# Kernel tuning notes

Hardware: AMD Instinct MI355X
Metric: run time of the kernel (lower is better)

The kernel has to match this reference:

```python
import jax, jax.numpy as jnp
import numpy as np

MAX_DELTAS = 4  # number of concurrently loaded delta adapters


def _dequant(qw, qz, sc):
    """GPTQ-style 4-bit dequant with a single group (g_idx == 0).

    qw: [D, O, K//8] int32, 8 x 4-bit values packed along the input (K) dim.
    qz: [D, O//8, 1] int32, 8 x 4-bit zero points packed along the output dim.
    sc: [D, O, 1] float scales (one group).
    Returns dense delta weights [D, O, K].
    """
    shifts = jnp.arange(8, dtype=jnp.int32) * 4
    D, O, Kp = qw.shape
    w = ((qw[:, :, :, None] >> shifts) & 0xF).reshape(D, O, Kp * 8)   # [D,O,K]
    z = ((qz[:, :, 0][:, :, None] >> shifts) & 0xF).reshape(D, O)     # [D,O]
    return (w.astype(sc.dtype) - (z.astype(sc.dtype) + 1.0)[:, :, None]) * sc


def setup_inputs() -> dict:
    key = jax.random.key(0)
    ks = jax.random.split(key, 16)
    T, IN = 1024, 4096
    Q, KV = 4096, 1024  # 32 q-heads, 8 kv-heads, head_size 128
    OUT = Q + 2 * KV    # 6144
    D, PACK = MAX_DELTAS, 8
    IMAX = np.int32(2**31 - 1)
    return {
        "x": jax.random.normal(ks[0], (T, IN), dtype=jnp.float32),
        "w_base": jax.random.normal(ks[1], (OUT, IN), dtype=jnp.float32) * 0.02,
        "bias": jax.random.normal(ks[2], (OUT,), dtype=jnp.float32) * 0.02,
        "qweight_q": jax.random.randint(ks[3], (D, Q, IN // PACK), 0, IMAX, dtype=jnp.int32),
        "qweight_k": jax.random.randint(ks[4], (D, KV, IN // PACK), 0, IMAX, dtype=jnp.int32),
        "qweight_v": jax.random.randint(ks[5], (D, KV, IN // PACK), 0, IMAX, dtype=jnp.int32),
        "qzeros_q": jax.random.randint(ks[6], (D, Q // PACK, 1), 0, IMAX, dtype=jnp.int32),
        "qzeros_k": jax.random.randint(ks[7], (D, KV // PACK, 1), 0, IMAX, dtype=jnp.int32),
        "qzeros_v": jax.random.randint(ks[8], (D, KV // PACK, 1), 0, IMAX, dtype=jnp.int32),
        "scales_q": jax.random.uniform(ks[9], (D, Q, 1), dtype=jnp.float32) * 0.01,
        "scales_k": jax.random.uniform(ks[10], (D, KV, 1), dtype=jnp.float32) * 0.01,
        "scales_v": jax.random.uniform(ks[11], (D, KV, 1), dtype=jnp.float32) * 0.01,
        "indices": jax.random.randint(ks[12], (T,), 0, D, dtype=jnp.int32),
    }


def reference(x, w_base, bias, qweight_q, qweight_k, qweight_v,
              qzeros_q, qzeros_k, qzeros_v, scales_q, scales_k, scales_v,
              indices):
    # Base fused QKV projection.
    out = x @ w_base.T + bias  # [T, OUT]
    # Dequantize the three packed delta stacks and concatenate along out dim,
    # matching the (q, k, v) output_slices scatter of apply_delta.
    Wd = jnp.concatenate([
        _dequant(qweight_q, qzeros_q, scales_q),
        _dequant(qweight_k, qzeros_k, scales_k),
        _dequant(qweight_v, qzeros_v, scales_v),
    ], axis=1)  # [D, OUT, IN]
    # Per-token indexed delta matmul: token t uses adapter indices[t].
    for d in range(MAX_DELTAS):
        xm = jnp.where((indices == d)[:, None], x, 0.0)  # [T, IN]
        out = out + xm @ Wd[d].T
    return out
```

## Files before the change

kernel.cpp:

```cpp
#include <hip/hip_runtime.h>
#include <stdint.h>

#define T_TOK 1024
#define K_IN  4096
#define N_OUT 6144
#define N_Q   4096
#define N_KV  1024
#define N_D   4
#define KP    512

#define TM 128
#define TN 128
#define BK 64
#define KSPLIT 2
#define KHALF (K_IN / KSPLIT)
#define PM_MAX 1536
#define MT (PM_MAX/TM)
#define NT (N_OUT/TN)

typedef __attribute__((ext_vector_type(8)))  short  short8;
typedef __attribute__((ext_vector_type(4)))  float  float4v;

__device__ __forceinline__ ushort f2bf(float f) {
    uint32_t u = __float_as_uint(f);
    u = (u + 0x7FFFu + ((u >> 16) & 1u)) >> 16;
    return (ushort)u;
}
__device__ __forceinline__ uint pack2(ushort a, ushort b) {
    return (uint)a | ((uint)b << 16);
}

__global__ void build_perm_kernel(const int* __restrict__ indices,
                                  int* __restrict__ perm,
                                  int* __restrict__ pofs) {
    __shared__ int cnt[N_D], cur[N_D], ps[N_D + 1];
    int tid = threadIdx.x;
    if (tid < N_D) { cnt[tid] = 0; cur[tid] = 0; }
    __syncthreads();
    for (int t = tid; t < T_TOK; t += blockDim.x) atomicAdd(&cnt[indices[t]], 1);
    for (int p = tid; p < PM_MAX; p += blockDim.x) perm[p] = -1;
    __syncthreads();
    if (tid == 0) {
        int run = 0;
        for (int d = 0; d < N_D; d++) { ps[d] = run; run += ((cnt[d] + TM - 1) / TM) * TM; }
        ps[N_D] = run;
        for (int d = 0; d <= N_D; d++) pofs[d] = ps[d];
    }
    __syncthreads();
    for (int t = tid; t < T_TOK; t += blockDim.x) {
        int d = indices[t];
        int r = atomicAdd(&cur[d], 1);
        perm[ps[d] + r] = t;
    }
}

__global__ void dequant_wall_kernel(const float* __restrict__ w_base,
                                    const int* __restrict__ qw_q, const int* __restrict__ qw_k, const int* __restrict__ qw_v,
                                    const int* __restrict__ qz_q, const int* __restrict__ qz_k, const int* __restrict__ qz_v,
                                    const float* __restrict__ sc_q, const float* __restrict__ sc_k, const float* __restrict__ sc_v,
                                    ushort* __restrict__ wall) {
    int id  = blockIdx.x * blockDim.x + threadIdx.x;
    int kq  = id & (KP - 1);
    int o   = id >> 9;

    const int* qw; const int* qz; const float* sc; int r, Osec;
    if (o < N_Q)            { qw = qw_q; qz = qz_q; sc = sc_q; r = o;                Osec = N_Q;  }
    else if (o < N_Q + N_KV){ qw = qw_k; qz = qz_k; sc = sc_k; r = o - N_Q;          Osec = N_KV; }
    else                    { qw = qw_v; qz = qz_v; sc = sc_v; r = o - (N_Q + N_KV); Osec = N_KV; }

    const float* wbp = w_base + (size_t)o * K_IN + (size_t)kq * 8;
    float4 wb0 = *(const float4*)(wbp);
    float4 wb1 = *(const float4*)(wbp + 4);
    float wb[8] = {wb0.x, wb0.y, wb0.z, wb0.w, wb1.x, wb1.y, wb1.z, wb1.w};

#pragma unroll
    for (int d = 0; d < N_D; d++) {
        int   q  = qw[((size_t)d * Osec + r) * KP + kq];
        int   zq = qz[(size_t)d * (Osec / 8) + (r >> 3)];
        float s  = sc[(size_t)d * Osec + r];
        float zs = (float)(((zq >> ((r & 7) * 4)) & 0xF) + 1) * s;

        ushort res[8];
#pragma unroll
        for (int j = 0; j < 8; j++) {
            float v = wb[j] + (float)((q >> (4 * j)) & 0xF) * s - zs;
            res[j] = f2bf(v);
        }
        uint4 packv;
        packv.x = pack2(res[0], res[1]); packv.y = pack2(res[2], res[3]);
        packv.z = pack2(res[4], res[5]); packv.w = pack2(res[6], res[7]);
        *(uint4*)(wall + ((size_t)d * N_OUT + o) * K_IN + (size_t)kq * 8) = packv;
    }
}

__global__ void build_xp_kernel(const float* __restrict__ x,
                                const int* __restrict__ perm,
                                ushort* __restrict__ xp) {
    int pm = blockIdx.x;
    int c0 = blockIdx.y * 2048 + threadIdx.x * 8;
    int tok = perm[pm];
    ushort res[8];
    if (tok < 0) {
#pragma unroll
        for (int j = 0; j < 8; j++) res[j] = 0;
    } else {
        const float* src = x + (size_t)tok * K_IN + c0;
#pragma unroll
        for (int j = 0; j < 8; j++) res[j] = f2bf(src[j]);
    }
    uint4 packv;
    packv.x = pack2(res[0], res[1]); packv.y = pack2(res[2], res[3]);
    packv.z = pack2(res[4], res[5]); packv.w = pack2(res[6], res[7]);
    *(uint4*)(xp + (size_t)pm * K_IN + c0) = packv;
}

__global__ void init_out_kernel(const float* __restrict__ bias,
                                float* __restrict__ out) {
    int id = blockIdx.x * blockDim.x + threadIdx.x;
    int n4 = id & (N_OUT / 4 - 1);
    int t  = id / (N_OUT / 4);
    float4 b = *(const float4*)(bias + n4 * 4);
    *(float4*)(out + (size_t)t * N_OUT + n4 * 4) = b;
}

__global__ __launch_bounds__(256, 4) void gemm_kernel(
    const ushort* __restrict__ xp, const ushort* __restrict__ wall,
    const int* __restrict__ perm, const int* __restrict__ pofs,
    float* __restrict__ out) {

    __shared__ ushort As[TM * BK];
    __shared__ ushort Bs[TN * BK];

    int bn = blockIdx.x, bm = blockIdx.y, kz = blockIdx.z;
    int m0 = bm * TM, n0 = bn * TN;
    int ptot = pofs[N_D];
    if (m0 >= ptot) return;
    int d = 0;
    while (d < N_D - 1 && m0 >= pofs[d + 1]) d++;

    const ushort* wsec = wall + (size_t)d * N_OUT * K_IN;

    int tid  = threadIdx.x;
    int lane = tid & 63;
    int wv   = tid >> 6;
    int wm   = (wv & 1) * 64;
    int wn   = (wv >> 1) * 64;
    int quad = lane >> 4;
    int l16  = lane & 15;
    int xa   = l16 & 7;

    const float4v zero4 = {0.f, 0.f, 0.f, 0.f};
    float4v acc[4][4];
#pragma unroll
    for (int i = 0; i < 4; i++)
#pragma unroll
        for (int j = 0; j < 4; j++) acc[i][j] = zero4;

    int kbase = kz * KHALF;
    for (int k0 = kbase; k0 < kbase + KHALF; k0 += BK) {
#pragma unroll
        for (int w = 0; w < 4; w++) {
            int p   = w * 256 + tid;
            int row = p >> 3;
            int ckl = (p & 7) ^ (row & 7);
            const ushort* ga = xp   + (size_t)(m0 + row) * K_IN + k0 + ckl * 8;
            const ushort* gb = wsec + (size_t)(n0 + row) * K_IN + k0 + ckl * 8;
            int base = (w * 256 + (tid & ~63)) * 8;
            __builtin_amdgcn_global_load_lds((const __attribute__((address_space(1))) void*)ga,
                                             (__attribute__((address_space(3))) void*)(As + base), 16, 0, 0);
            __builtin_amdgcn_global_load_lds((const __attribute__((address_space(1))) void*)gb,
                                             (__attribute__((address_space(3))) void*)(Bs + base), 16, 0, 0);
        }
        __syncthreads();

#pragma unroll
        for (int kk = 0; kk < BK; kk += 32) {
            int ckb = (kk >> 3) + quad;
            short8 a[4], b[4];
#pragma unroll
            for (int i = 0; i < 4; i++)
                a[i] = *(const short8*)(As + (wm + i * 16 + l16) * BK + (ckb ^ xa) * 8);
#pragma unroll
            for (int j = 0; j < 4; j++)
                b[j] = *(const short8*)(Bs + (wn + j * 16 + l16) * BK + (ckb ^ xa) * 8);
#pragma unroll
            for (int i = 0; i < 4; i++)
#pragma unroll
                for (int j = 0; j < 4; j++)
                    acc[i][j] = __builtin_amdgcn_mfma_f32_16x16x32_bf16(a[i], b[j], acc[i][j], 0, 0, 0);
        }
        __syncthreads();
    }

#pragma unroll
    for (int i = 0; i < 4; i++) {
        int toks[4];
#pragma unroll
        for (int r = 0; r < 4; r++) toks[r] = perm[m0 + wm + i * 16 + quad * 4 + r];
#pragma unroll
        for (int j = 0; j < 4; j++) {
            int col = n0 + wn + j * 16 + l16;
#pragma unroll
            for (int r = 0; r < 4; r++) {
                int tok = toks[r];
                if (tok >= 0) atomicAdd(out + (size_t)tok * N_OUT + col, acc[i][j][r]);
            }
        }
    }
}

extern "C" void kernel_launch(void* const* d_in, const int* in_sizes, int n_in,
                              void* d_out, int out_size, void* d_ws, size_t ws_size,
                              hipStream_t stream) {
    const float* x      = (const float*)d_in[0];
    const float* w_base = (const float*)d_in[1];
    const float* bias   = (const float*)d_in[2];
    const int*   qw_q   = (const int*)d_in[3];
    const int*   qw_k   = (const int*)d_in[4];
    const int*   qw_v   = (const int*)d_in[5];
    const int*   qz_q   = (const int*)d_in[6];
    const int*   qz_k   = (const int*)d_in[7];
    const int*   qz_v   = (const int*)d_in[8];
    const float* sc_q   = (const float*)d_in[9];
    const float* sc_k   = (const float*)d_in[10];
    const float* sc_v   = (const float*)d_in[11];
    const int*   indices= (const int*)d_in[12];
    float* out = (float*)d_out;

    char* ws = (char*)d_ws;
    ushort* wall = (ushort*)ws;
    size_t wall_bytes = (size_t)N_D * N_OUT * K_IN * 2;
    ushort* xp = (ushort*)(ws + wall_bytes);
    size_t xp_bytes = (size_t)PM_MAX * K_IN * 2;
    int* perm = (int*)(ws + wall_bytes + xp_bytes);
    int* pofs = perm + PM_MAX;

    build_perm_kernel<<<1, 256, 0, stream>>>(indices, perm, pofs);
    dequant_wall_kernel<<<(N_OUT * KP) / 256, 256, 0, stream>>>(
        w_base, qw_q, qw_k, qw_v, qz_q, qz_k, qz_v, sc_q, sc_k, sc_v, wall);
    build_xp_kernel<<<dim3(PM_MAX, 2), 256, 0, stream>>>(x, perm, xp);
    init_out_kernel<<<(T_TOK * N_OUT / 4) / 256, 256, 0, stream>>>(bias, out);
    gemm_kernel<<<dim3(NT, MT, KSPLIT), 256, 0, stream>>>(xp, wall, perm, pofs, out);
}
```

Baseline: 376.9 us.

## Double-buffer GEMM LDS tiles, swizzle block order, use nontemporal loads

The GEMM now stages the next K-tile into a second LDS buffer while computing on the current one, which halves barriers per step and overlaps global loads with MFMA work. The grid is flattened and remapped so groups of 8 adjacent N-tiles are scheduled together for L2 reuse of activation tiles. The dequant and activation-cast kernels use nontemporal loads for streamed inputs. LDS usage doubles, so occupancy is lowered to 2 blocks per CU.

```diff
diff --git a/kernel.cpp b/kernel.cpp
--- a/kernel.cpp
+++ b/kernel.cpp
@@ -14,12 +14,16 @@
 #define BK 64
 #define KSPLIT 2
 #define KHALF (K_IN / KSPLIT)
+#define NSTEPS (KHALF / BK)
 #define PM_MAX 1536
 #define MT (PM_MAX/TM)
 #define NT (N_OUT/TN)
+#define NBLK (NT * MT * KSPLIT)
 
 typedef __attribute__((ext_vector_type(8)))  short  short8;
 typedef __attribute__((ext_vector_type(4)))  float  float4v;
+typedef __attribute__((ext_vector_type(4)))  float  f32x4;
+typedef __attribute__((ext_vector_type(4)))  uint   u32x4;
 
 __device__ __forceinline__ ushort f2bf(float f) {
     uint32_t u = __float_as_uint(f);
@@ -68,14 +72,14 @@
     else if (o < N_Q + N_KV){ qw = qw_k; qz = qz_k; sc = sc_k; r = o - N_Q;          Osec = N_KV; }
     else                    { qw = qw_v; qz = qz_v; sc = sc_v; r = o - (N_Q + N_KV); Osec = N_KV; }
 
-    const float* wbp = w_base + (size_t)o * K_IN + (size_t)kq * 8;
-    float4 wb0 = *(const float4*)(wbp);
-    float4 wb1 = *(const float4*)(wbp + 4);
+    const f32x4* wbp = (const f32x4*)(w_base + (size_t)o * K_IN + (size_t)kq * 8);
+    f32x4 wb0 = __builtin_nontemporal_load(wbp);
+    f32x4 wb1 = __builtin_nontemporal_load(wbp + 1);
     float wb[8] = {wb0.x, wb0.y, wb0.z, wb0.w, wb1.x, wb1.y, wb1.z, wb1.w};
 
 #pragma unroll
     for (int d = 0; d < N_D; d++) {
-        int   q  = qw[((size_t)d * Osec + r) * KP + kq];
+        int   q  = __builtin_nontemporal_load(qw + ((size_t)d * Osec + r) * KP + kq);
         int   zq = qz[(size_t)d * (Osec / 8) + (r >> 3)];
         float s  = sc[(size_t)d * Osec + r];
         float zs = (float)(((zq >> ((r & 7) * 4)) & 0xF) + 1) * s;
@@ -86,10 +90,10 @@
             float v = wb[j] + (float)((q >> (4 * j)) & 0xF) * s - zs;
             res[j] = f2bf(v);
         }
-        uint4 packv;
+        u32x4 packv;
         packv.x = pack2(res[0], res[1]); packv.y = pack2(res[2], res[3]);
         packv.z = pack2(res[4], res[5]); packv.w = pack2(res[6], res[7]);
-        *(uint4*)(wall + ((size_t)d * N_OUT + o) * K_IN + (size_t)kq * 8) = packv;
+        *(u32x4*)(wall + ((size_t)d * N_OUT + o) * K_IN + (size_t)kq * 8) = packv;
     }
 }
 
@@ -104,14 +108,17 @@
 #pragma unroll
         for (int j = 0; j < 8; j++) res[j] = 0;
     } else {
-        const float* src = x + (size_t)tok * K_IN + c0;
-#pragma unroll
-        for (int j = 0; j < 8; j++) res[j] = f2bf(src[j]);
-    }
-    uint4 packv;
+        const f32x4* src = (const f32x4*)(x + (size_t)tok * K_IN + c0);
+        f32x4 a = __builtin_nontemporal_load(src);
+        f32x4 b = __builtin_nontemporal_load(src + 1);
+        float v[8] = {a.x, a.y, a.z, a.w, b.x, b.y, b.z, b.w};
+#pragma unroll
+        for (int j = 0; j < 8; j++) res[j] = f2bf(v[j]);
+    }
+    u32x4 packv;
     packv.x = pack2(res[0], res[1]); packv.y = pack2(res[2], res[3]);
     packv.z = pack2(res[4], res[5]); packv.w = pack2(res[6], res[7]);
-    *(uint4*)(xp + (size_t)pm * K_IN + c0) = packv;
+    *(u32x4*)(xp + (size_t)pm * K_IN + c0) = packv;
 }
 
 __global__ void init_out_kernel(const float* __restrict__ bias,
@@ -123,15 +130,20 @@
     *(float4*)(out + (size_t)t * N_OUT + n4 * 4) = b;
 }
 
-__global__ __launch_bounds__(256, 4) void gemm_kernel(
+__global__ __launch_bounds__(256, 2) void gemm_kernel(
     const ushort* __restrict__ xp, const ushort* __restrict__ wall,
     const int* __restrict__ perm, const int* __restrict__ pofs,
     float* __restrict__ out) {
 
-    __shared__ ushort As[TM * BK];
-    __shared__ ushort Bs[TN * BK];
-
-    int bn = blockIdx.x, bm = blockIdx.y, kz = blockIdx.z;
+    __shared__ ushort As[2][TM * BK];
+    __shared__ ushort Bs[2][TN * BK];
+
+    int lin  = blockIdx.x;
+    int low3 = lin & 7, rest = lin >> 3;
+    int j    = rest % 24, bq = rest / 24;
+    int bn   = bq * 8 + low3;
+    int bm   = j % MT, kz = j / MT;
+
     int m0 = bm * TM, n0 = bn * TN;
     int ptot = pofs[N_D];
     if (m0 >= ptot) return;
@@ -154,10 +166,9 @@
 #pragma unroll
     for (int i = 0; i < 4; i++)
 #pragma unroll
-        for (int j = 0; j < 4; j++) acc[i][j] = zero4;
-
-    int kbase = kz * KHALF;
-    for (int k0 = kbase; k0 < kbase + KHALF; k0 += BK) {
+        for (int jj = 0; jj < 4; jj++) acc[i][jj] = zero4;
+
+    auto stage = [&](ushort* dstA, ushort* dstB, int k0) {
 #pragma unroll
         for (int w = 0; w < 4; w++) {
             int p   = w * 256 + tid;
@@ -167,29 +178,40 @@
             const ushort* gb = wsec + (size_t)(n0 + row) * K_IN + k0 + ckl * 8;
             int base = (w * 256 + (tid & ~63)) * 8;
             __builtin_amdgcn_global_load_lds((const __attribute__((address_space(1))) void*)ga,
-                                             (__attribute__((address_space(3))) void*)(As + base), 16, 0, 0);
+                                             (__attribute__((address_space(3))) void*)(dstA + base), 16, 0, 0);
             __builtin_amdgcn_global_load_lds((const __attribute__((address_space(1))) void*)gb,
-                                             (__attribute__((address_space(3))) void*)(Bs + base), 16, 0, 0);
-        }
-        __syncthreads();
-
+                                             (__attribute__((address_space(3))) void*)(dstB + base), 16, 0, 0);
+        }
+    };
+
+    int kbase = kz * KHALF;
+    int buf = 0;
+    stage(As[0], Bs[0], kbase);
+    __syncthreads();
+
+    for (int s = 0; s < NSTEPS; s++) {
+        if (s + 1 < NSTEPS) stage(As[1 - buf], Bs[1 - buf], kbase + (s + 1) * BK);
+
+        const ushort* Ab = As[buf];
+        const ushort* Bb = Bs[buf];
 #pragma unroll
         for (int kk = 0; kk < BK; kk += 32) {
             int ckb = (kk >> 3) + quad;
             short8 a[4], b[4];
 #pragma unroll
             for (int i = 0; i < 4; i++)
-                a[i] = *(const short8*)(As + (wm + i * 16 + l16) * BK + (ckb ^ xa) * 8);
-#pragma unroll
-            for (int j = 0; j < 4; j++)
-                b[j] = *(const short8*)(Bs + (wn + j * 16 + l16) * BK + (ckb ^ xa) * 8);
+                a[i] = *(const short8*)(Ab + (wm + i * 16 + l16) * BK + (ckb ^ xa) * 8);
+#pragma unroll
+            for (int jj = 0; jj < 4; jj++)
+                b[jj] = *(const short8*)(Bb + (wn + jj * 16 + l16) * BK + (ckb ^ xa) * 8);
 #pragma unroll
             for (int i = 0; i < 4; i++)
 #pragma unroll
-                for (int j = 0; j < 4; j++)
-                    acc[i][j] = __builtin_amdgcn_mfma_f32_16x16x32_bf16(a[i], b[j], acc[i][j], 0, 0, 0);
+                for (int jj = 0; jj < 4; jj++)
+                    acc[i][jj] = __builtin_amdgcn_mfma_f32_16x16x32_bf16(a[i], b[jj], acc[i][jj], 0, 0, 0);
         }
         __syncthreads();
+        buf ^= 1;
     }
 
 #pragma unroll
@@ -198,12 +220,12 @@
 #pragma unroll
         for (int r = 0; r < 4; r++) toks[r] = perm[m0 + wm + i * 16 + quad * 4 + r];
 #pragma unroll
-        for (int j = 0; j < 4; j++) {
-            int col = n0 + wn + j * 16 + l16;
+        for (int jj = 0; jj < 4; jj++) {
+            int col = n0 + wn + jj * 16 + l16;
 #pragma unroll
             for (int r = 0; r < 4; r++) {
                 int tok = toks[r];
-                if (tok >= 0) atomicAdd(out + (size_t)tok * N_OUT + col, acc[i][j][r]);
+                if (tok >= 0) atomicAdd(out + (size_t)tok * N_OUT + col, acc[i][jj][r]);
             }
         }
     }
@@ -240,5 +262,5 @@
         w_base, qw_q, qw_k, qw_v, qz_q, qz_k, qz_v, sc_q, sc_k, sc_v, wall);
     build_xp_kernel<<<dim3(PM_MAX, 2), 256, 0, stream>>>(x, perm, xp);
     init_out_kernel<<<(T_TOK * N_OUT / 4) / 256, 256, 0, stream>>>(bias, out);
-    gemm_kernel<<<dim3(NT, MT, KSPLIT), 256, 0, stream>>>(xp, wall, perm, pofs, out);
-}
+    gemm_kernel<<<NBLK, 256, 0, stream>>>(xp, wall, perm, pofs, out);
+}
```

Result: faster. 367.9 us (-2.4%).
